# Performance work log

Measured on AMD Instinct MI355X. Metric: run time of the kernel, lower is better.

## Reference

```python
import jax, jax.numpy as jnp
import numpy as np

N_NODES = 50000


def setup_inputs() -> dict:
    key = jax.random.key(0)
    ks = jax.random.split(key, 8)
    d = 64
    n_edges = 800000
    h = 256
    in_dim = 3 * d  # in-agg + out-agg + node feat
    return {
        "node_feat": jax.random.normal(ks[0], (N_NODES, d), dtype=jnp.float32),
        "edge_feat": jax.random.normal(ks[1], (n_edges, d), dtype=jnp.float32),
        "senders": jax.random.randint(ks[2], (n_edges,), 0, N_NODES, dtype=jnp.int32),
        "receivers": jax.random.randint(ks[3], (n_edges,), 0, N_NODES, dtype=jnp.int32),
        "W1": jax.random.normal(ks[4], (in_dim, h), dtype=jnp.float32) * (1.0 / np.sqrt(in_dim)),
        "b1": jnp.zeros((h,), dtype=jnp.float32),
        "W2": jax.random.normal(ks[5], (h, d), dtype=jnp.float32) * (1.0 / np.sqrt(h)),
        "b2": jnp.zeros((d,), dtype=jnp.float32),
    }


def reference(node_feat, edge_feat, senders, receivers, W1, b1, W2, b2):
    # Incoming edges of node v are edges whose receiver == v; outgoing: sender == v.
    # Sum-aggregate edge features per node (replaces the per-node Python gather loop).
    in_agg = jax.ops.segment_sum(edge_feat, receivers, num_segments=N_NODES)   # [N, d]
    out_agg = jax.ops.segment_sum(edge_feat, senders, num_segments=N_NODES)    # [N, d]
    # cat(in_aggregated + out_aggregated, dim=1) then cat with vertex data per node
    upd_in = jnp.concatenate([in_agg, out_agg, node_feat], axis=1)              # [N, 3d]
    # Shared MLP updater for vertex type 'node'
    hcat = jax.nn.relu(upd_in @ W1 + b1)
    return hcat @ W2 + b2                                                       # [N, d]
```

## Files before the change

### kernel.cpp

```cpp
#include <hip/hip_runtime.h>

#define D 64
#define IN_DIM 192
#define H 256
#define NB 64
#define BLK 256
#define MBLK 512
#define SCAN_BLK 512


__global__ void zero_kernel(int* __restrict__ p, int n) {
    int i = blockIdx.x * blockDim.x + threadIdx.x;
    for (; i < n; i += gridDim.x * blockDim.x) p[i] = 0;
}

__global__ void hist_kernel(const int* __restrict__ senders,
                            const int* __restrict__ receivers,
                            int* __restrict__ deg, int n_edges, int N) {
    int e = blockIdx.x * blockDim.x + threadIdx.x;
    if (e >= n_edges) return;
    atomicAdd(&deg[receivers[e]], 1);
    atomicAdd(&deg[N + senders[e]], 1);
}

__global__ void scan_a_kernel(const int* __restrict__ deg, int* __restrict__ off,
                              int* __restrict__ bsums, int n) {
    __shared__ int s[SCAN_BLK];
    int t = threadIdx.x;
    int gid = blockIdx.x * SCAN_BLK + t;
    int v = (gid < n) ? deg[gid] : 0;
    s[t] = v;
    for (int ofs = 1; ofs < SCAN_BLK; ofs <<= 1) {
        __syncthreads();
        int x = (t >= ofs) ? s[t - ofs] : 0;
        __syncthreads();
        s[t] += x;
    }
    __syncthreads();
    if (gid < n) off[gid] = s[t] - v;
    if (t == SCAN_BLK - 1) bsums[blockIdx.x] = s[t];
}

__global__ void scan_b_kernel(int* __restrict__ bsums, int nb) {
    __shared__ int s[256];
    int t = threadIdx.x;
    int v = (t < nb) ? bsums[t] : 0;
    s[t] = v;
    for (int ofs = 1; ofs < 256; ofs <<= 1) {
        __syncthreads();
        int x = (t >= ofs) ? s[t - ofs] : 0;
        __syncthreads();
        s[t] += x;
    }
    __syncthreads();
    if (t < nb) bsums[t] = s[t] - v;
}

__global__ void scan_c_kernel(int* __restrict__ off, const int* __restrict__ bsums, int n) {
    int gid = blockIdx.x * SCAN_BLK + threadIdx.x;
    if (gid < n) off[gid] += bsums[blockIdx.x];
}

__global__ void fill_kernel(const int* __restrict__ senders,
                            const int* __restrict__ receivers,
                            const int* __restrict__ off,
                            int* __restrict__ cursor,
                            int* __restrict__ elist, int n_edges, int N) {
    int e = blockIdx.x * blockDim.x + threadIdx.x;
    if (e >= n_edges) return;
    int r = receivers[e];
    int p = atomicAdd(&cursor[r], 1);
    elist[off[r] + p] = e;
    int sd = senders[e];
    int q = atomicAdd(&cursor[N + sd], 1);
    elist[off[N + sd] + q] = e;
}

__global__ void gather_kernel(const float* __restrict__ edge_feat,
                              const float* __restrict__ node_feat,
                              const int* __restrict__ off,
                              const int* __restrict__ elist,
                              float* __restrict__ X, int N, int totE2) {
    int lane = threadIdx.x & 63;
    int seg = blockIdx.x * 4 + (threadIdx.x >> 6);
    if (seg >= 2 * N) return;
    int beg = off[seg];
    int end = (seg + 1 < 2 * N) ? off[seg + 1] : totE2;
    const int sub = lane >> 4;
    const int c4  = lane & 15;

    float4 a0 = make_float4(0.f, 0.f, 0.f, 0.f);
    float4 a1 = make_float4(0.f, 0.f, 0.f, 0.f);
    int i = beg + sub;
    for (; i + 4 < end; i += 8) {
        int e0 = elist[i];
        int e1 = elist[i + 4];
        const float4 v0 = *(const float4*)(edge_feat + (size_t)e0 * D + c4 * 4);
        const float4 v1 = *(const float4*)(edge_feat + (size_t)e1 * D + c4 * 4);
        a0.x += v0.x; a0.y += v0.y; a0.z += v0.z; a0.w += v0.w;
        a1.x += v1.x; a1.y += v1.y; a1.z += v1.z; a1.w += v1.w;
    }
    if (i < end) {
        int e = elist[i];
        const float4 v = *(const float4*)(edge_feat + (size_t)e * D + c4 * 4);
        a0.x += v.x; a0.y += v.y; a0.z += v.z; a0.w += v.w;
    }
    float4 a;
    a.x = a0.x + a1.x; a.y = a0.y + a1.y; a.z = a0.z + a1.z; a.w = a0.w + a1.w;
    a.x += __shfl_xor(a.x, 16); a.y += __shfl_xor(a.y, 16);
    a.z += __shfl_xor(a.z, 16); a.w += __shfl_xor(a.w, 16);
    a.x += __shfl_xor(a.x, 32); a.y += __shfl_xor(a.y, 32);
    a.z += __shfl_xor(a.z, 32); a.w += __shfl_xor(a.w, 32);

    if (seg < N) {
        float* row = X + (size_t)seg * IN_DIM;
        if (lane < 16) *(float4*)(row + 4 * c4) = a;
        row[128 + lane] = node_feat[(size_t)seg * D + lane];
    } else {
        if (lane < 16)
            *(float4*)(X + (size_t)(seg - N) * IN_DIM + D + 4 * c4) = a;
    }
}

#define XS_STRIDE 196
#define HS_STRIDE 260
#define SMEM_BYTES 132096

__device__ __forceinline__ void fma_row(float a, const float4 w, float* acc4) {
    acc4[0] = fmaf(a, w.x, acc4[0]);
    acc4[1] = fmaf(a, w.y, acc4[1]);
    acc4[2] = fmaf(a, w.z, acc4[2]);
    acc4[3] = fmaf(a, w.w, acc4[3]);
}

__global__ __launch_bounds__(MBLK, 2) void mlp_kernel(
    const float* __restrict__ X,
    const float* __restrict__ W1, const float* __restrict__ b1,
    const float* __restrict__ W2, const float* __restrict__ b2,
    float* __restrict__ out, int N) {
    __shared__ __align__(16) char smem_raw[SMEM_BYTES];
    float* Xs  = (float*)smem_raw;
    float* W1s = (float*)(smem_raw + 50176);
    float* Hs  = (float*)smem_raw;
    float* W2s = (float*)(smem_raw + 66560);

    const int t = threadIdx.x;
    const int n0 = blockIdx.x * NB;

    #pragma unroll
    for (int q = 0; q < 8; ++q) {
        int idx = t + q * MBLK;
        *(float4*)(W2s + idx * 4) = *(const float4*)(W2 + idx * 4);
    }

    for (int idx = t; idx < NB * 48; idx += MBLK) {
        int n = idx / 48;
        int c4 = idx - n * 48;
        int node = n0 + n;
        float4 v = make_float4(0.f, 0.f, 0.f, 0.f);
        if (node < N) v = *(const float4*)(X + (size_t)node * IN_DIM + c4 * 4);
        *(float4*)(Xs + n * XS_STRIDE + c4 * 4) = v;
    }

    const int tc = t & 31;
    const int tn = t >> 5;

    float acc[4][8];
    {
        float4 bA = *(const float4*)(b1 + 4 * tc);
        float4 bB = *(const float4*)(b1 + 128 + 4 * tc);
        #pragma unroll
        for (int i = 0; i < 4; ++i) {
            acc[i][0] = bA.x; acc[i][1] = bA.y; acc[i][2] = bA.z; acc[i][3] = bA.w;
            acc[i][4] = bB.x; acc[i][5] = bB.y; acc[i][6] = bB.z; acc[i][7] = bB.w;
        }
    }

    for (int k0 = 0; k0 < IN_DIM; k0 += 16) {
        __syncthreads();
        #pragma unroll
        for (int q = 0; q < 2; ++q) {
            int idx = t + q * MBLK;
            int kk = idx >> 6;
            int cc = (idx & 63) << 2;
            *(float4*)(W1s + kk * H + cc) = *(const float4*)(W1 + (size_t)(k0 + kk) * H + cc);
        }
        __syncthreads();
        #pragma unroll
        for (int k = 0; k < 16; k += 4) {
            float4 xv[4];
            #pragma unroll
            for (int i = 0; i < 4; ++i)
                xv[i] = *(const float4*)(Xs + (tn * 4 + i) * XS_STRIDE + k0 + k);
            float4 wA[4], wB[4];
            #pragma unroll
            for (int kk = 0; kk < 4; ++kk) {
                wA[kk] = *(const float4*)(W1s + (k + kk) * H + 4 * tc);
                wB[kk] = *(const float4*)(W1s + (k + kk) * H + 128 + 4 * tc);
            }
            #pragma unroll
            for (int i = 0; i < 4; ++i) {
                fma_row(xv[i].x, wA[0], &acc[i][0]); fma_row(xv[i].x, wB[0], &acc[i][4]);
                fma_row(xv[i].y, wA[1], &acc[i][0]); fma_row(xv[i].y, wB[1], &acc[i][4]);
                fma_row(xv[i].z, wA[2], &acc[i][0]); fma_row(xv[i].z, wB[2], &acc[i][4]);
                fma_row(xv[i].w, wA[3], &acc[i][0]); fma_row(xv[i].w, wB[3], &acc[i][4]);
            }
        }
    }

    __syncthreads();

    #pragma unroll
    for (int i = 0; i < 4; ++i) {
        float4 a, b;
        a.x = fmaxf(acc[i][0], 0.f); a.y = fmaxf(acc[i][1], 0.f);
        a.z = fmaxf(acc[i][2], 0.f); a.w = fmaxf(acc[i][3], 0.f);
        b.x = fmaxf(acc[i][4], 0.f); b.y = fmaxf(acc[i][5], 0.f);
        b.z = fmaxf(acc[i][6], 0.f); b.w = fmaxf(acc[i][7], 0.f);
        *(float4*)(Hs + (tn * 4 + i) * HS_STRIDE + 4 * tc) = a;
        *(float4*)(Hs + (tn * 4 + i) * HS_STRIDE + 128 + 4 * tc) = b;
    }
    __syncthreads();

    const int tc2 = t & 15;
    const int tn2 = t >> 4;
    float4 o[2];
    {
        float4 bb = *(const float4*)(b2 + 4 * tc2);
        o[0] = bb; o[1] = bb;
    }
    #pragma unroll 4
    for (int k = 0; k < H; k += 4) {
        float4 h[2], w[4];
        #pragma unroll
        for (int i = 0; i < 2; ++i)
            h[i] = *(const float4*)(Hs + (tn2 * 2 + i) * HS_STRIDE + k);
        #pragma unroll
        for (int kk = 0; kk < 4; ++kk)
            w[kk] = *(const float4*)(W2s + (k + kk) * D + 4 * tc2);
        #pragma unroll
        for (int i = 0; i < 2; ++i) {
            fma_row(h[i].x, w[0], (float*)&o[i]);
            fma_row(h[i].y, w[1], (float*)&o[i]);
            fma_row(h[i].z, w[2], (float*)&o[i]);
            fma_row(h[i].w, w[3], (float*)&o[i]);
        }
    }
    #pragma unroll
    for (int i = 0; i < 2; ++i) {
        int node = n0 + tn2 * 2 + i;
        if (node < N)
            *(float4*)(out + (size_t)node * D + 4 * tc2) = o[i];
    }
}

extern "C" void kernel_launch(void* const* d_in, const int* in_sizes, int n_in,
                              void* d_out, int out_size, void* d_ws, size_t ws_size,
                              hipStream_t stream) {
    const float* node_feat = (const float*)d_in[0];
    const float* edge_feat = (const float*)d_in[1];
    const int*   senders   = (const int*)d_in[2];
    const int*   receivers = (const int*)d_in[3];
    const float* W1        = (const float*)d_in[4];
    const float* b1        = (const float*)d_in[5];
    const float* W2        = (const float*)d_in[6];
    const float* b2        = (const float*)d_in[7];
    float* out = (float*)d_out;

    const int N       = in_sizes[0] / D;
    const int n_edges = in_sizes[2];
    const int totE2   = 2 * n_edges;
    const int n2      = 2 * N;

    float* X    = (float*)d_ws;
    int* deg    = (int*)(X + (size_t)N * IN_DIM);
    int* cursor = deg + n2;
    int* off    = cursor + n2;
    int* bsums  = off + n2;
    int* elist  = bsums + 256;

    zero_kernel<<<196, BLK, 0, stream>>>(deg, 2 * n2);
    hist_kernel<<<(n_edges + BLK - 1) / BLK, BLK, 0, stream>>>(
        senders, receivers, deg, n_edges, N);
    int nb = (n2 + SCAN_BLK - 1) / SCAN_BLK;
    scan_a_kernel<<<nb, SCAN_BLK, 0, stream>>>(deg, off, bsums, n2);
    scan_b_kernel<<<1, 256, 0, stream>>>(bsums, nb);
    scan_c_kernel<<<nb, SCAN_BLK, 0, stream>>>(off, bsums, n2);
    fill_kernel<<<(n_edges + BLK - 1) / BLK, BLK, 0, stream>>>(
        senders, receivers, off, cursor, elist, n_edges, N);
    gather_kernel<<<(n2 + 3) / 4, BLK, 0, stream>>>(
        edge_feat, node_feat, off, elist, X, N, totE2);
    mlp_kernel<<<(N + NB - 1) / NB, MBLK, 0, stream>>>(X, W1, b1, W2, b2, out, N);
}
```

Before: 667.2 us.

## Run node MLP on bf16 MFMA with bf16 activations and pre-transposed weights

Replaces the fp32 FMA tiled MLP with a kernel that uses 16x16x32 bf16 MFMA instructions for both layers. The hidden activations are staged in shared memory as bf16. The gather kernel now writes the concatenated node input as bf16, which halves that intermediate's traffic. A small new kernel converts and transposes W1 and W2 to bf16 each call so MFMA operands load directly from global memory. This trades fp32 accuracy for bf16 rounding of inputs, weights and hidden activations. The last block also reads rows past N from the workspace.

```diff
diff --git a/kernel.cpp b/kernel.cpp
--- a/kernel.cpp
+++ b/kernel.cpp
@@ -1,12 +1,21 @@
 #include <hip/hip_runtime.h>
+#include <hip/hip_bf16.h>
 
 #define D 64
 #define IN_DIM 192
 #define H 256
 #define NB 64
 #define BLK 256
-#define MBLK 512
 #define SCAN_BLK 512
+#define HPAD 280
+
+typedef __attribute__((ext_vector_type(8))) short bf16x8;
+typedef __attribute__((ext_vector_type(4))) float f32x4;
+
+static __device__ __forceinline__ ushort f2b(float x) {
+    __hip_bfloat16 hb = __float2bfloat16(x);
+    return *reinterpret_cast<ushort*>(&hb);
+}
 
 
 __global__ void zero_kernel(int* __restrict__ p, int n) {
@@ -76,11 +85,26 @@
     elist[off[N + sd] + q] = e;
 }
 
+__global__ void convw_kernel(const float* __restrict__ W1,
+                             const float* __restrict__ W2,
+                             ushort* __restrict__ W1T,
+                             ushort* __restrict__ W2T) {
+    int i = blockIdx.x * BLK + threadIdx.x;
+    if (i < 49152) {
+        int h = i / IN_DIM, k = i - h * IN_DIM;
+        W1T[i] = f2b(W1[(size_t)k * H + h]);
+    } else if (i < 49152 + 16384) {
+        int j = i - 49152;
+        int d = j / H, hh = j - d * H;
+        W2T[j] = f2b(W2[(size_t)hh * D + d]);
+    }
+}
+
 __global__ void gather_kernel(const float* __restrict__ edge_feat,
                               const float* __restrict__ node_feat,
                               const int* __restrict__ off,
                               const int* __restrict__ elist,
-                              float* __restrict__ X, int N, int totE2) {
+                              ushort* __restrict__ Xb, int N, int totE2) {
     int lane = threadIdx.x & 63;
     int seg = blockIdx.x * 4 + (threadIdx.x >> 6);
     if (seg >= 2 * N) return;
@@ -112,145 +136,93 @@
     a.x += __shfl_xor(a.x, 32); a.y += __shfl_xor(a.y, 32);
     a.z += __shfl_xor(a.z, 32); a.w += __shfl_xor(a.w, 32);
 
+    ushort4 ub;
+    ub.x = f2b(a.x); ub.y = f2b(a.y); ub.z = f2b(a.z); ub.w = f2b(a.w);
+
     if (seg < N) {
-        float* row = X + (size_t)seg * IN_DIM;
-        if (lane < 16) *(float4*)(row + 4 * c4) = a;
-        row[128 + lane] = node_feat[(size_t)seg * D + lane];
+        ushort* row = Xb + (size_t)seg * IN_DIM;
+        if (lane < 16) *(ushort4*)(row + 4 * c4) = ub;
+        row[128 + lane] = f2b(node_feat[(size_t)seg * D + lane]);
     } else {
         if (lane < 16)
-            *(float4*)(X + (size_t)(seg - N) * IN_DIM + D + 4 * c4) = a;
-    }
-}
-
-#define XS_STRIDE 196
-#define HS_STRIDE 260
-#define SMEM_BYTES 132096
-
-__device__ __forceinline__ void fma_row(float a, const float4 w, float* acc4) {
-    acc4[0] = fmaf(a, w.x, acc4[0]);
-    acc4[1] = fmaf(a, w.y, acc4[1]);
-    acc4[2] = fmaf(a, w.z, acc4[2]);
-    acc4[3] = fmaf(a, w.w, acc4[3]);
-}
-
-__global__ __launch_bounds__(MBLK, 2) void mlp_kernel(
-    const float* __restrict__ X,
-    const float* __restrict__ W1, const float* __restrict__ b1,
-    const float* __restrict__ W2, const float* __restrict__ b2,
+            *(ushort4*)(Xb + (size_t)(seg - N) * IN_DIM + D + 4 * c4) = ub;
+    }
+}
+
+__global__ __launch_bounds__(BLK, 4) void mlp_mfma_kernel(
+    const ushort* __restrict__ Xb,
+    const ushort* __restrict__ W1T, const float* __restrict__ b1,
+    const ushort* __restrict__ W2T, const float* __restrict__ b2,
     float* __restrict__ out, int N) {
-    __shared__ __align__(16) char smem_raw[SMEM_BYTES];
-    float* Xs  = (float*)smem_raw;
-    float* W1s = (float*)(smem_raw + 50176);
-    float* Hs  = (float*)smem_raw;
-    float* W2s = (float*)(smem_raw + 66560);
+    __shared__ __align__(16) ushort Hs[64 * HPAD];
 
     const int t = threadIdx.x;
-    const int n0 = blockIdx.x * NB;
-
-    #pragma unroll
-    for (int q = 0; q < 8; ++q) {
-        int idx = t + q * MBLK;
-        *(float4*)(W2s + idx * 4) = *(const float4*)(W2 + idx * 4);
-    }
-
-    for (int idx = t; idx < NB * 48; idx += MBLK) {
-        int n = idx / 48;
-        int c4 = idx - n * 48;
-        int node = n0 + n;
-        float4 v = make_float4(0.f, 0.f, 0.f, 0.f);
-        if (node < N) v = *(const float4*)(X + (size_t)node * IN_DIM + c4 * 4);
-        *(float4*)(Xs + n * XS_STRIDE + c4 * 4) = v;
-    }
-
-    const int tc = t & 31;
-    const int tn = t >> 5;
-
-    float acc[4][8];
-    {
-        float4 bA = *(const float4*)(b1 + 4 * tc);
-        float4 bB = *(const float4*)(b1 + 128 + 4 * tc);
-        #pragma unroll
-        for (int i = 0; i < 4; ++i) {
-            acc[i][0] = bA.x; acc[i][1] = bA.y; acc[i][2] = bA.z; acc[i][3] = bA.w;
-            acc[i][4] = bB.x; acc[i][5] = bB.y; acc[i][6] = bB.z; acc[i][7] = bB.w;
-        }
-    }
-
-    for (int k0 = 0; k0 < IN_DIM; k0 += 16) {
-        __syncthreads();
-        #pragma unroll
-        for (int q = 0; q < 2; ++q) {
-            int idx = t + q * MBLK;
-            int kk = idx >> 6;
-            int cc = (idx & 63) << 2;
-            *(float4*)(W1s + kk * H + cc) = *(const float4*)(W1 + (size_t)(k0 + kk) * H + cc);
-        }
-        __syncthreads();
-        #pragma unroll
-        for (int k = 0; k < 16; k += 4) {
-            float4 xv[4];
-            #pragma unroll
-            for (int i = 0; i < 4; ++i)
-                xv[i] = *(const float4*)(Xs + (tn * 4 + i) * XS_STRIDE + k0 + k);
-            float4 wA[4], wB[4];
-            #pragma unroll
-            for (int kk = 0; kk < 4; ++kk) {
-                wA[kk] = *(const float4*)(W1s + (k + kk) * H + 4 * tc);
-                wB[kk] = *(const float4*)(W1s + (k + kk) * H + 128 + 4 * tc);
-            }
-            #pragma unroll
-            for (int i = 0; i < 4; ++i) {
-                fma_row(xv[i].x, wA[0], &acc[i][0]); fma_row(xv[i].x, wB[0], &acc[i][4]);
-                fma_row(xv[i].y, wA[1], &acc[i][0]); fma_row(xv[i].y, wB[1], &acc[i][4]);
-                fma_row(xv[i].z, wA[2], &acc[i][0]); fma_row(xv[i].z, wB[2], &acc[i][4]);
-                fma_row(xv[i].w, wA[3], &acc[i][0]); fma_row(xv[i].w, wB[3], &acc[i][4]);
-            }
-        }
-    }
-
+    const int lane = t & 63;
+    const int w = t >> 6;
+    const int lr = lane & 15;
+    const int lk = lane >> 4;
+    const int nodeBase = blockIdx.x * NB + w * 16;
+
+    f32x4 acc[16];
+    #pragma unroll
+    for (int c = 0; c < 16; ++c) acc[c] = (f32x4){0.f, 0.f, 0.f, 0.f};
+
+    bf16x8 afr[6];
+    const ushort* xrow = Xb + (size_t)(nodeBase + lr) * IN_DIM + lk * 8;
+    #pragma unroll
+    for (int ks = 0; ks < 6; ++ks)
+        afr[ks] = *(const bf16x8*)(xrow + ks * 32);
+
+    #pragma unroll
+    for (int c = 0; c < 16; ++c) {
+        const ushort* wcol = W1T + (size_t)(c * 16 + lr) * IN_DIM + lk * 8;
+        #pragma unroll
+        for (int ks = 0; ks < 6; ++ks) {
+            bf16x8 bfr = *(const bf16x8*)(wcol + ks * 32);
+            acc[c] = __builtin_amdgcn_mfma_f32_16x16x32_bf16(afr[ks], bfr, acc[c], 0, 0, 0);
+        }
+    }
+
+    #pragma unroll
+    for (int c = 0; c < 16; ++c) {
+        float bv = b1[c * 16 + lr];
+        #pragma unroll
+        for (int r = 0; r < 4; ++r) {
+            float h = fmaxf(acc[c][r] + bv, 0.f);
+            int row = w * 16 + lk * 4 + r;
+            Hs[row * HPAD + c * 16 + lr] = f2b(h);
+        }
+    }
     __syncthreads();
 
-    #pragma unroll
-    for (int i = 0; i < 4; ++i) {
-        float4 a, b;
-        a.x = fmaxf(acc[i][0], 0.f); a.y = fmaxf(acc[i][1], 0.f);
-        a.z = fmaxf(acc[i][2], 0.f); a.w = fmaxf(acc[i][3], 0.f);
-        b.x = fmaxf(acc[i][4], 0.f); b.y = fmaxf(acc[i][5], 0.f);
-        b.z = fmaxf(acc[i][6], 0.f); b.w = fmaxf(acc[i][7], 0.f);
-        *(float4*)(Hs + (tn * 4 + i) * HS_STRIDE + 4 * tc) = a;
-        *(float4*)(Hs + (tn * 4 + i) * HS_STRIDE + 128 + 4 * tc) = b;
-    }
-    __syncthreads();
-
-    const int tc2 = t & 15;
-    const int tn2 = t >> 4;
-    float4 o[2];
-    {
-        float4 bb = *(const float4*)(b2 + 4 * tc2);
-        o[0] = bb; o[1] = bb;
-    }
-    #pragma unroll 4
-    for (int k = 0; k < H; k += 4) {
-        float4 h[2], w[4];
-        #pragma unroll
-        for (int i = 0; i < 2; ++i)
-            h[i] = *(const float4*)(Hs + (tn2 * 2 + i) * HS_STRIDE + k);
-        #pragma unroll
-        for (int kk = 0; kk < 4; ++kk)
-            w[kk] = *(const float4*)(W2s + (k + kk) * D + 4 * tc2);
-        #pragma unroll
-        for (int i = 0; i < 2; ++i) {
-            fma_row(h[i].x, w[0], (float*)&o[i]);
-            fma_row(h[i].y, w[1], (float*)&o[i]);
-            fma_row(h[i].z, w[2], (float*)&o[i]);
-            fma_row(h[i].w, w[3], (float*)&o[i]);
-        }
-    }
-    #pragma unroll
-    for (int i = 0; i < 2; ++i) {
-        int node = n0 + tn2 * 2 + i;
-        if (node < N)
-            *(float4*)(out + (size_t)node * D + 4 * tc2) = o[i];
+    bf16x8 a2[8];
+    #pragma unroll
+    for (int ks = 0; ks < 8; ++ks)
+        a2[ks] = *(const bf16x8*)(&Hs[(w * 16 + lr) * HPAD + ks * 32 + lk * 8]);
+
+    f32x4 acc2[4];
+    #pragma unroll
+    for (int c = 0; c < 4; ++c) acc2[c] = (f32x4){0.f, 0.f, 0.f, 0.f};
+
+    #pragma unroll
+    for (int c = 0; c < 4; ++c) {
+        const ushort* wcol = W2T + (size_t)(c * 16 + lr) * H + lk * 8;
+        #pragma unroll
+        for (int ks = 0; ks < 8; ++ks) {
+            bf16x8 bfr = *(const bf16x8*)(wcol + ks * 32);
+            acc2[c] = __builtin_amdgcn_mfma_f32_16x16x32_bf16(a2[ks], bfr, acc2[c], 0, 0, 0);
+        }
+    }
+
+    #pragma unroll
+    for (int c = 0; c < 4; ++c) {
+        float bv = b2[c * 16 + lr];
+        #pragma unroll
+        for (int r = 0; r < 4; ++r) {
+            int node = nodeBase + lk * 4 + r;
+            if (node < N)
+                out[(size_t)node * D + c * 16 + lr] = acc2[c][r] + bv;
+        }
     }
 }
 
@@ -272,12 +244,14 @@
     const int totE2   = 2 * n_edges;
     const int n2      = 2 * N;
 
-    float* X    = (float*)d_ws;
-    int* deg    = (int*)(X + (size_t)N * IN_DIM);
-    int* cursor = deg + n2;
-    int* off    = cursor + n2;
-    int* bsums  = off + n2;
-    int* elist  = bsums + 256;
+    ushort* Xb   = (ushort*)d_ws;
+    int* deg     = (int*)(Xb + (size_t)N * IN_DIM);
+    int* cursor  = deg + n2;
+    int* off     = cursor + n2;
+    int* bsums   = off + n2;
+    int* elist   = bsums + 256;
+    ushort* W1T  = (ushort*)(elist + totE2);
+    ushort* W2T  = W1T + 49152;
 
     zero_kernel<<<196, BLK, 0, stream>>>(deg, 2 * n2);
     hist_kernel<<<(n_edges + BLK - 1) / BLK, BLK, 0, stream>>>(
@@ -288,7 +262,10 @@
     scan_c_kernel<<<nb, SCAN_BLK, 0, stream>>>(off, bsums, n2);
     fill_kernel<<<(n_edges + BLK - 1) / BLK, BLK, 0, stream>>>(
         senders, receivers, off, cursor, elist, n_edges, N);
+    convw_kernel<<<(49152 + 16384 + BLK - 1) / BLK, BLK, 0, stream>>>(
+        W1, W2, W1T, W2T);
     gather_kernel<<<(n2 + 3) / 4, BLK, 0, stream>>>(
-        edge_feat, node_feat, off, elist, X, N, totE2);
-    mlp_kernel<<<(N + NB - 1) / NB, MBLK, 0, stream>>>(X, W1, b1, W2, b2, out, N);
-}
+        edge_feat, node_feat, off, elist, Xb, N, totE2);
+    mlp_mfma_kernel<<<(N + NB - 1) / NB, BLK, 0, stream>>>(
+        Xb, W1T, b1, W2T, b2, out, N);
+}
```

Result: faster. 596.7 us (-10.6%).
